# Performance work log

Hardware: AMD Instinct MI355X
Metric: run time of the kernel (lower is better)

The kernel has to match this reference:

```python
import jax, jax.numpy as jnp
import numpy as np

N_NODES = 50000
N_EDGES = 800000
N_GRAPHS = 128
IN_C, HID_C, OUT_C = 128, 256, 128


def setup_inputs() -> dict:
    key = jax.random.key(0)
    ks = jax.random.split(key, 10)
    x = jax.random.normal(ks[0], (N_NODES, IN_C), dtype=jnp.float32)
    edge_index = jax.random.randint(ks[1], (2, N_EDGES), 0, N_NODES, dtype=jnp.int32)
    batch = jnp.sort(jax.random.randint(ks[2], (N_NODES,), 0, N_GRAPHS, dtype=jnp.int32))
    def glorot(k, fan_in, fan_out):
        lim = (6.0 / (fan_in + fan_out)) ** 0.5
        return jax.random.uniform(k, (fan_in, fan_out), jnp.float32, -lim, lim)
    W1 = glorot(ks[3], IN_C, HID_C)
    b1 = jnp.zeros((HID_C,), jnp.float32)
    W2 = glorot(ks[4], HID_C, HID_C)
    b2 = jnp.zeros((HID_C,), jnp.float32)
    Wfc = glorot(ks[5], HID_C, OUT_C)
    bfc = jnp.zeros((OUT_C,), jnp.float32)
    return {"x": x, "edge_index": edge_index, "batch": batch,
            "W1": W1, "b1": b1, "W2": W2, "b2": b2, "Wfc": Wfc, "bfc": bfc}


def _gcn_conv(x, src, dst, W, b, n_nodes):
    # PyG GCNConv: h = x @ W; out[dst] += norm * h[src]; out += b
    h = x @ W  # [N, F_out]
    ones = jnp.ones(src.shape, dtype=h.dtype)
    deg = jax.ops.segment_sum(ones, dst, num_segments=n_nodes)  # in-degree incl self loops
    dinv = jnp.where(deg > 0, jax.lax.rsqrt(deg), 0.0)
    norm = dinv[src] * dinv[dst]                    # [E]
    msg = h[src] * norm[:, None]                    # gather + scale, [E, F_out]
    out = jax.ops.segment_sum(msg, dst, num_segments=n_nodes)  # scatter-add
    return out + b


def reference(x, edge_index, batch, W1, b1, W2, b2, Wfc, bfc):
    n = x.shape[0]
    loops = jnp.arange(n, dtype=edge_index.dtype)
    src = jnp.concatenate([edge_index[0], loops])   # add self loops (GCNConv default)
    dst = jnp.concatenate([edge_index[1], loops])
    h = jax.nn.relu(_gcn_conv(x, src, dst, W1, b1, n))
    h = jax.nn.relu(_gcn_conv(h, src, dst, W2, b2, n))
    # global_mean_pool keyed by batch index
    sums = jax.ops.segment_sum(h, batch, num_segments=N_GRAPHS)          # [G, HID]
    cnts = jax.ops.segment_sum(jnp.ones((n,), h.dtype), batch, num_segments=N_GRAPHS)
    pooled = sums / jnp.maximum(cnts, 1.0)[:, None]
    return pooled @ Wfc + bfc
```

## Files before the change

kernel.cpp:

```cpp
#include <hip/hip_runtime.h>
#include <type_traits>

#define HID 256
#define INC 128
#define OUTC 128

typedef __attribute__((ext_vector_type(8))) short short8;
typedef __attribute__((ext_vector_type(4))) float floatx4;

__device__ __forceinline__ unsigned short f2bf(float f) {
    unsigned int u = __float_as_uint(f);
    unsigned int r = (u + 0x7FFFu + ((u >> 16) & 1u)) >> 16;
    return (unsigned short)r;
}

__device__ __forceinline__ void bfacc2(float* a, uint u, float nr) {
    a[0] = fmaf(nr, __uint_as_float(u << 16), a[0]);
    a[1] = fmaf(nr, __uint_as_float(u & 0xFFFF0000u), a[1]);
}

__global__ void k_hist(const int* __restrict__ dst, int* __restrict__ cnt, int e) {
    int i = blockIdx.x * blockDim.x + threadIdx.x;
    if (i < e) atomicAdd(&cnt[dst[i]], 1);
}

__global__ __launch_bounds__(256) void k_scan_local(const int* __restrict__ cnt,
                                                    int* __restrict__ ex, int* __restrict__ blk_sum,
                                                    float* __restrict__ dinv, int n) {
    __shared__ int s[256];
    const int t = threadIdx.x;
    const int i = blockIdx.x * 256 + t;
    const int v = (i < n) ? cnt[i] : 0;
    if (i < n) dinv[i] = rsqrtf((float)v + 1.0f);
    s[t] = v;
    __syncthreads();
    for (int off = 1; off < 256; off <<= 1) {
        int add = (t >= off) ? s[t - off] : 0;
        __syncthreads();
        s[t] += add;
        __syncthreads();
    }
    if (i < n) ex[i] = s[t] - v;
    if (t == 255) blk_sum[blockIdx.x] = s[255];
}

__global__ __launch_bounds__(256) void k_scan_add(int* __restrict__ row_ptr,
                                                  const int* __restrict__ blk_sum,
                                                  int* __restrict__ cnt, int n, int e) {
    __shared__ int s[256];
    const int t = threadIdx.x;
    const int b = blockIdx.x;
    s[t] = (t < b) ? blk_sum[t] : 0;
    __syncthreads();
    for (int off = 128; off > 0; off >>= 1) {
        if (t < off) s[t] += s[t + off];
        __syncthreads();
    }
    const int offset = s[0];
    const int i = b * 256 + t;
    if (i < n) { row_ptr[i] += offset; cnt[i] = 0; }
    if (i == 0) row_ptr[n] = e;
}

__global__ void k_fill(const int* __restrict__ src, const int* __restrict__ dst,
                       const int* __restrict__ row_ptr, int* __restrict__ cursor,
                       int2* __restrict__ csr, const float* __restrict__ dinv, int e) {
    int i = blockIdx.x * blockDim.x + threadIdx.x;
    if (i < e) {
        const int d = dst[i];
        const int s = src[i];
        const int pos = row_ptr[d] + atomicAdd(&cursor[d], 1);
        csr[pos] = make_int2(s, __float_as_int(dinv[s] * dinv[d]));
    }
}

__global__ void k_conv(const float* __restrict__ x, unsigned short* __restrict__ xb,
                       const float* __restrict__ W1, unsigned short* __restrict__ Wt1,
                       const float* __restrict__ W2, unsigned short* __restrict__ Wt2,
                       int* __restrict__ cnt, float* __restrict__ pooled,
                       int nx4, int n) {
    const int id = blockIdx.x * 256 + threadIdx.x;
    if (id < n) cnt[id] = 0;
    if (id < 128 * HID) pooled[id] = 0.0f;
    if (id < nx4) {
        const float4 v = *(const float4*)(x + (size_t)id * 4);
        uint2 o;
        o.x = (unsigned)f2bf(v.x) | ((unsigned)f2bf(v.y) << 16);
        o.y = (unsigned)f2bf(v.z) | ((unsigned)f2bf(v.w) << 16);
        *(uint2*)(xb + (size_t)id * 4) = o;
        return;
    }
    const int id2 = id - nx4;
    if (id2 < INC * HID) {
        const int nn = id2 / INC;
        const int kk = id2 - nn * INC;
        Wt1[id2] = f2bf(W1[kk * HID + nn]);
        return;
    }
    const int id3 = id2 - INC * HID;
    if (id3 < HID * HID) {
        const int nn = id3 / HID;
        const int kk = id3 - nn * HID;
        Wt2[id3] = f2bf(W2[kk * HID + nn]);
    }
}

template <int CH>
__global__ __launch_bounds__(256) void k_agg(const unsigned short* __restrict__ h,
                                             const int* __restrict__ row_ptr,
                                             const int2* __restrict__ csr,
                                             const float* __restrict__ dinv,
                                             unsigned short* __restrict__ out, int n) {
    constexpr int CPL = CH / 64;
    using VT = std::conditional_t<CPL == 2, uint, uint2>;
    const int v = (blockIdx.x * 256 + threadIdx.x) >> 6;
    const int lane = threadIdx.x & 63;
    if (v >= n) return;
    const float dv = dinv[v];
    const unsigned short* hl = h + lane * CPL;

    float acc[CPL];
    {
        const VT u = *(const VT*)(hl + (size_t)v * CH);
        const float s2 = dv * dv;
        if constexpr (CPL == 2) {
            acc[0] = s2 * __uint_as_float(((uint)u) << 16);
            acc[1] = s2 * __uint_as_float(((uint)u) & 0xFFFF0000u);
        } else {
            const uint2 w = (uint2)u;
            acc[0] = s2 * __uint_as_float(w.x << 16);
            acc[1] = s2 * __uint_as_float(w.x & 0xFFFF0000u);
            acc[2] = s2 * __uint_as_float(w.y << 16);
            acc[3] = s2 * __uint_as_float(w.y & 0xFFFF0000u);
        }
    }

    const int beg = row_ptr[v];
    const int end = row_ptr[v + 1];
    int i = beg;
    for (; i + 4 <= end; i += 4) {
        const int2 p0 = csr[i];
        const int2 p1 = csr[i + 1];
        const int2 p2 = csr[i + 2];
        const int2 p3 = csr[i + 3];
        const float n0 = __int_as_float(p0.y);
        const float n1 = __int_as_float(p1.y);
        const float n2 = __int_as_float(p2.y);
        const float n3 = __int_as_float(p3.y);
        const VT r0 = *(const VT*)(hl + (size_t)p0.x * CH);
        const VT r1 = *(const VT*)(hl + (size_t)p1.x * CH);
        const VT r2 = *(const VT*)(hl + (size_t)p2.x * CH);
        const VT r3 = *(const VT*)(hl + (size_t)p3.x * CH);
        if constexpr (CPL == 2) {
            bfacc2(acc, (uint)r0, n0);
            bfacc2(acc, (uint)r1, n1);
            bfacc2(acc, (uint)r2, n2);
            bfacc2(acc, (uint)r3, n3);
        } else {
            const uint2 w0 = (uint2)r0, w1 = (uint2)r1, w2 = (uint2)r2, w3 = (uint2)r3;
            bfacc2(acc, w0.x, n0); bfacc2(acc + 2, w0.y, n0);
            bfacc2(acc, w1.x, n1); bfacc2(acc + 2, w1.y, n1);
            bfacc2(acc, w2.x, n2); bfacc2(acc + 2, w2.y, n2);
            bfacc2(acc, w3.x, n3); bfacc2(acc + 2, w3.y, n3);
        }
    }
    for (; i < end; ++i) {
        const int2 p0 = csr[i];
        const float n0 = __int_as_float(p0.y);
        const VT r0 = *(const VT*)(hl + (size_t)p0.x * CH);
        if constexpr (CPL == 2) {
            bfacc2(acc, (uint)r0, n0);
        } else {
            const uint2 w0 = (uint2)r0;
            bfacc2(acc, w0.x, n0); bfacc2(acc + 2, w0.y, n0);
        }
    }

    if constexpr (CPL == 2) {
        uint o = (unsigned)f2bf(acc[0]) | ((unsigned)f2bf(acc[1]) << 16);
        *(uint*)(out + (size_t)v * CH + lane * CPL) = o;
    } else {
        uint2 o;
        o.x = (unsigned)f2bf(acc[0]) | ((unsigned)f2bf(acc[1]) << 16);
        o.y = (unsigned)f2bf(acc[2]) | ((unsigned)f2bf(acc[3]) << 16);
        *(uint2*)(out + (size_t)v * CH + lane * CPL) = o;
    }
}

template <int K, bool RELU, bool POOL, typename OT>
__global__ __launch_bounds__(256) void k_gemm_mfma(const unsigned short* __restrict__ A,
                                                   const unsigned short* __restrict__ Wt,
                                                   const float* __restrict__ bias,
                                                   OT* __restrict__ out,
                                                   const int* __restrict__ batch,
                                                   float* __restrict__ pooled_sum, int M) {
    constexpr int LDA = K + 8;
    __shared__ unsigned short sA[32 * LDA];
    __shared__ int s_batch[32];
    const int t = threadIdx.x;
    const int row0 = blockIdx.x * 32;

    {
        const int r = t >> 3;
        const int c0 = (t & 7) * (K / 8);
        unsigned short* dstp = &sA[r * LDA + c0];
        if (row0 + r < M) {
            const unsigned short* srcp = A + (size_t)(row0 + r) * K + c0;
#pragma unroll
            for (int j = 0; j < K / 8; j += 8)
                *(uint4*)(dstp + j) = *(const uint4*)(srcp + j);
        } else {
            const uint4 z = {0, 0, 0, 0};
#pragma unroll
            for (int j = 0; j < K / 8; j += 8) *(uint4*)(dstp + j) = z;
        }
        if constexpr (POOL) {
            if (t < 32) s_batch[t] = (row0 + t < M) ? batch[row0 + t] : -1;
        }
    }
    __syncthreads();

    const int wv = t >> 6;
    const int lane = t & 63;
    const int m16 = lane & 15;
    const int quad = lane >> 4;

    floatx4 acc[2][4];
#pragma unroll
    for (int h2 = 0; h2 < 2; ++h2)
#pragma unroll
        for (int j = 0; j < 4; ++j) acc[h2][j] = (floatx4){0.f, 0.f, 0.f, 0.f};

    const unsigned short* ap0 = &sA[m16 * LDA + quad * 8];
    const unsigned short* ap1 = &sA[(16 + m16) * LDA + quad * 8];
    const unsigned short* bp = Wt + (size_t)(wv * 64 + m16) * K + quad * 8;

#pragma unroll
    for (int k0 = 0; k0 < K; k0 += 32) {
        const short8 a0 = *(const short8*)(ap0 + k0);
        const short8 a1 = *(const short8*)(ap1 + k0);
        const short8 b0 = *(const short8*)(bp + 0 * 16 * K + k0);
        const short8 b1 = *(const short8*)(bp + 1 * 16 * K + k0);
        const short8 b2 = *(const short8*)(bp + 2 * 16 * K + k0);
        const short8 b3 = *(const short8*)(bp + 3 * 16 * K + k0);
        acc[0][0] = __builtin_amdgcn_mfma_f32_16x16x32_bf16(a0, b0, acc[0][0], 0, 0, 0);
        acc[0][1] = __builtin_amdgcn_mfma_f32_16x16x32_bf16(a0, b1, acc[0][1], 0, 0, 0);
        acc[0][2] = __builtin_amdgcn_mfma_f32_16x16x32_bf16(a0, b2, acc[0][2], 0, 0, 0);
        acc[0][3] = __builtin_amdgcn_mfma_f32_16x16x32_bf16(a0, b3, acc[0][3], 0, 0, 0);
        acc[1][0] = __builtin_amdgcn_mfma_f32_16x16x32_bf16(a1, b0, acc[1][0], 0, 0, 0);
        acc[1][1] = __builtin_amdgcn_mfma_f32_16x16x32_bf16(a1, b1, acc[1][1], 0, 0, 0);
        acc[1][2] = __builtin_amdgcn_mfma_f32_16x16x32_bf16(a1, b2, acc[1][2], 0, 0, 0);
        acc[1][3] = __builtin_amdgcn_mfma_f32_16x16x32_bf16(a1, b3, acc[1][3], 0, 0, 0);
    }

    const int nbase = wv * 64 + m16;
    const float bb0 = bias[nbase + 0];
    const float bb1 = bias[nbase + 16];
    const float bb2 = bias[nbase + 32];
    const float bb3 = bias[nbase + 48];

    if constexpr (POOL) {
        float ps0 = 0.f, ps1 = 0.f, ps2 = 0.f, ps3 = 0.f;
        int gcur = -1;
#pragma unroll
        for (int h2 = 0; h2 < 2; ++h2) {
#pragma unroll
            for (int j = 0; j < 4; ++j) {
                const int rl = h2 * 16 + quad * 4 + j;
                const int g = s_batch[rl];
                if (g < 0) continue;
                if (g != gcur) {
                    if (gcur >= 0) {
                        float* pp = pooled_sum + gcur * HID + nbase;
                        atomicAdd(pp + 0, ps0);
                        atomicAdd(pp + 16, ps1);
                        atomicAdd(pp + 32, ps2);
                        atomicAdd(pp + 48, ps3);
                    }
                    ps0 = ps1 = ps2 = ps3 = 0.f;
                    gcur = g;
                }
                ps0 += fmaxf(acc[h2][0][j] + bb0, 0.f);
                ps1 += fmaxf(acc[h2][1][j] + bb1, 0.f);
                ps2 += fmaxf(acc[h2][2][j] + bb2, 0.f);
                ps3 += fmaxf(acc[h2][3][j] + bb3, 0.f);
            }
        }
        if (gcur >= 0) {
            float* pp = pooled_sum + gcur * HID + nbase;
            atomicAdd(pp + 0, ps0);
            atomicAdd(pp + 16, ps1);
            atomicAdd(pp + 32, ps2);
            atomicAdd(pp + 48, ps3);
        }
    } else {
#pragma unroll
        for (int h2 = 0; h2 < 2; ++h2) {
#pragma unroll
            for (int j = 0; j < 4; ++j) {
                const int row = row0 + h2 * 16 + quad * 4 + j;
                if (row >= M) continue;
                float v0 = acc[h2][0][j] + bb0;
                float v1 = acc[h2][1][j] + bb1;
                float v2 = acc[h2][2][j] + bb2;
                float v3 = acc[h2][3][j] + bb3;
                if constexpr (RELU) {
                    v0 = fmaxf(v0, 0.f); v1 = fmaxf(v1, 0.f);
                    v2 = fmaxf(v2, 0.f); v3 = fmaxf(v3, 0.f);
                }
                out[(size_t)row * HID + nbase + 0]  = (OT)f2bf(v0);
                out[(size_t)row * HID + nbase + 16] = (OT)f2bf(v1);
                out[(size_t)row * HID + nbase + 32] = (OT)f2bf(v2);
                out[(size_t)row * HID + nbase + 48] = (OT)f2bf(v3);
            }
        }
    }
}

__global__ void k_fc(const float* __restrict__ pooled_sum, const int* __restrict__ batch,
                     const float* __restrict__ W, const float* __restrict__ b,
                     float* __restrict__ out, int n) {
    const int g = blockIdx.x;
    const int c = threadIdx.x;
    int a = 0, hi = n;
    while (a < hi) { int m = (a + hi) >> 1; if (batch[m] < g) a = m + 1; else hi = m; }
    const int start = a;
    hi = n;
    while (a < hi) { int m = (a + hi) >> 1; if (batch[m] < g + 1) a = m + 1; else hi = m; }
    const float cnt = (float)(a - start);

    float acc = 0.0f;
    const float* p = pooled_sum + g * HID;
    for (int k = 0; k < HID; ++k) acc += p[k] * W[k * OUTC + c];
    out[g * OUTC + c] = acc / fmaxf(cnt, 1.0f) + b[c];
}

extern "C" void kernel_launch(void* const* d_in, const int* in_sizes, int n_in,
                              void* d_out, int out_size, void* d_ws, size_t ws_size,
                              hipStream_t stream) {
    const float* x   = (const float*)d_in[0];
    const int*   ei  = (const int*)d_in[1];
    const int*   bat = (const int*)d_in[2];
    const float* W1  = (const float*)d_in[3];
    const float* b1  = (const float*)d_in[4];
    const float* W2  = (const float*)d_in[5];
    const float* b2  = (const float*)d_in[6];
    const float* Wfc = (const float*)d_in[7];
    const float* bfc = (const float*)d_in[8];
    float* out = (float*)d_out;

    const int n = in_sizes[2];
    const int e = in_sizes[1] / 2;
    const int* src = ei;
    const int* dst = ei + e;
    const int nb = (n + 255) / 256;

    size_t off = 0;
    auto alloc = [&](size_t bytes) {
        char* p = (char*)d_ws + off;
        off += (bytes + 255) & ~(size_t)255;
        return p;
    };
    int*   cnt     = (int*)alloc((size_t)n * 4);
    int*   row_ptr = (int*)alloc((size_t)(n + 1) * 4);
    int*   blk_sum = (int*)alloc(512 * 4);
    int2*  csr     = (int2*)alloc((size_t)e * 8);
    float* dinv    = (float*)alloc((size_t)n * 4);
    unsigned short* Wt1 = (unsigned short*)alloc((size_t)INC * HID * 2);
    unsigned short* Wt2 = (unsigned short*)alloc((size_t)HID * HID * 2);
    unsigned short* R1  = (unsigned short*)alloc((size_t)n * HID * 2);
    unsigned short* R2  = (unsigned short*)alloc((size_t)n * INC * 2);
    unsigned short* R3  = (unsigned short*)alloc((size_t)n * HID * 2);
    float* pooled = (float*)alloc((size_t)128 * HID * 4);

    const int TB = 256;
    const int nx4 = n * INC / 4;

    k_conv<<<(nx4 + INC * HID + HID * HID + TB - 1) / TB, TB, 0, stream>>>(
        x, R1, W1, Wt1, W2, Wt2, cnt, pooled, nx4, n);

    k_hist<<<(e + TB - 1) / TB, TB, 0, stream>>>(dst, cnt, e);
    k_scan_local<<<nb, TB, 0, stream>>>(cnt, row_ptr, blk_sum, dinv, n);
    k_scan_add<<<nb, TB, 0, stream>>>(row_ptr, blk_sum, cnt, n, e);
    k_fill<<<(e + TB - 1) / TB, TB, 0, stream>>>(src, dst, row_ptr, cnt, csr, dinv, e);

    const int gemm_blocks = (n + 31) / 32;
    const int agg_blocks = (n + 3) / 4;

    k_agg<INC><<<agg_blocks, TB, 0, stream>>>(R1, row_ptr, csr, dinv, R2, n);
    k_gemm_mfma<INC, true, false, unsigned short><<<gemm_blocks, TB, 0, stream>>>(
        R2, Wt1, b1, R3, nullptr, nullptr, n);

    k_agg<HID><<<agg_blocks, TB, 0, stream>>>(R3, row_ptr, csr, dinv, R1, n);
    k_gemm_mfma<HID, true, true, float><<<gemm_blocks, TB, 0, stream>>>(
        R1, Wt2, b2, (float*)nullptr, bat, pooled, n);

    k_fc<<<128, 128, 0, stream>>>(pooled, bat, Wfc, bfc, out, n);
}
```

Baseline: 347.2 us.

## Use half-wave aggregation and persistent register-resident-weight MFMA GEMM

The aggregation kernel now assigns 32 lanes per node with wider vector loads, and handles the edge tail with clamped, zero-weighted padded iterations instead of a scalar remainder loop. The GEMM becomes a persistent grid of 512 blocks, each loading its weight fragments into registers once and looping over row tiles. A fragments are read directly from global memory rather than staged through shared memory, which removes the block-wide sync. This cuts per-tile reloads of the weights and the LDS traffic, at the cost of more register pressure (launch bounds 256,2) and uncoalesced direct A loads.

```diff
diff --git a/kernel.cpp b/kernel.cpp
--- a/kernel.cpp
+++ b/kernel.cpp
@@ -111,207 +111,215 @@
                                              const int2* __restrict__ csr,
                                              const float* __restrict__ dinv,
                                              unsigned short* __restrict__ out, int n) {
-    constexpr int CPL = CH / 64;
-    using VT = std::conditional_t<CPL == 2, uint, uint2>;
-    const int v = (blockIdx.x * 256 + threadIdx.x) >> 6;
-    const int lane = threadIdx.x & 63;
+    constexpr int CPL = CH / 32;
+    using VT = std::conditional_t<CPL == 4, uint2, uint4>;
+    const int v = (blockIdx.x * 256 + threadIdx.x) >> 5;
+    const int l = threadIdx.x & 31;
     if (v >= n) return;
     const float dv = dinv[v];
-    const unsigned short* hl = h + lane * CPL;
+    const unsigned short* hl = h + l * CPL;
 
     float acc[CPL];
     {
         const VT u = *(const VT*)(hl + (size_t)v * CH);
         const float s2 = dv * dv;
-        if constexpr (CPL == 2) {
-            acc[0] = s2 * __uint_as_float(((uint)u) << 16);
-            acc[1] = s2 * __uint_as_float(((uint)u) & 0xFFFF0000u);
-        } else {
+        if constexpr (CPL == 4) {
             const uint2 w = (uint2)u;
             acc[0] = s2 * __uint_as_float(w.x << 16);
             acc[1] = s2 * __uint_as_float(w.x & 0xFFFF0000u);
             acc[2] = s2 * __uint_as_float(w.y << 16);
             acc[3] = s2 * __uint_as_float(w.y & 0xFFFF0000u);
+        } else {
+            const uint4 w = (uint4)u;
+            acc[0] = s2 * __uint_as_float(w.x << 16);
+            acc[1] = s2 * __uint_as_float(w.x & 0xFFFF0000u);
+            acc[2] = s2 * __uint_as_float(w.y << 16);
+            acc[3] = s2 * __uint_as_float(w.y & 0xFFFF0000u);
+            acc[4] = s2 * __uint_as_float(w.z << 16);
+            acc[5] = s2 * __uint_as_float(w.z & 0xFFFF0000u);
+            acc[6] = s2 * __uint_as_float(w.w << 16);
+            acc[7] = s2 * __uint_as_float(w.w & 0xFFFF0000u);
         }
     }
 
     const int beg = row_ptr[v];
     const int end = row_ptr[v + 1];
-    int i = beg;
-    for (; i + 4 <= end; i += 4) {
+    for (int i = beg; i < end; i += 4) {
+        const int e1 = min(i + 1, end - 1);
+        const int e2 = min(i + 2, end - 1);
+        const int e3 = min(i + 3, end - 1);
         const int2 p0 = csr[i];
-        const int2 p1 = csr[i + 1];
-        const int2 p2 = csr[i + 2];
-        const int2 p3 = csr[i + 3];
+        const int2 p1 = csr[e1];
+        const int2 p2 = csr[e2];
+        const int2 p3 = csr[e3];
         const float n0 = __int_as_float(p0.y);
-        const float n1 = __int_as_float(p1.y);
-        const float n2 = __int_as_float(p2.y);
-        const float n3 = __int_as_float(p3.y);
+        const float n1 = (i + 1 < end) ? __int_as_float(p1.y) : 0.0f;
+        const float n2 = (i + 2 < end) ? __int_as_float(p2.y) : 0.0f;
+        const float n3 = (i + 3 < end) ? __int_as_float(p3.y) : 0.0f;
         const VT r0 = *(const VT*)(hl + (size_t)p0.x * CH);
         const VT r1 = *(const VT*)(hl + (size_t)p1.x * CH);
         const VT r2 = *(const VT*)(hl + (size_t)p2.x * CH);
         const VT r3 = *(const VT*)(hl + (size_t)p3.x * CH);
-        if constexpr (CPL == 2) {
-            bfacc2(acc, (uint)r0, n0);
-            bfacc2(acc, (uint)r1, n1);
-            bfacc2(acc, (uint)r2, n2);
-            bfacc2(acc, (uint)r3, n3);
-        } else {
+        if constexpr (CPL == 4) {
             const uint2 w0 = (uint2)r0, w1 = (uint2)r1, w2 = (uint2)r2, w3 = (uint2)r3;
             bfacc2(acc, w0.x, n0); bfacc2(acc + 2, w0.y, n0);
             bfacc2(acc, w1.x, n1); bfacc2(acc + 2, w1.y, n1);
             bfacc2(acc, w2.x, n2); bfacc2(acc + 2, w2.y, n2);
             bfacc2(acc, w3.x, n3); bfacc2(acc + 2, w3.y, n3);
+        } else {
+            const uint4 w0 = (uint4)r0, w1 = (uint4)r1, w2 = (uint4)r2, w3 = (uint4)r3;
+            bfacc2(acc, w0.x, n0); bfacc2(acc + 2, w0.y, n0);
+            bfacc2(acc + 4, w0.z, n0); bfacc2(acc + 6, w0.w, n0);
+            bfacc2(acc, w1.x, n1); bfacc2(acc + 2, w1.y, n1);
+            bfacc2(acc + 4, w1.z, n1); bfacc2(acc + 6, w1.w, n1);
+            bfacc2(acc, w2.x, n2); bfacc2(acc + 2, w2.y, n2);
+            bfacc2(acc + 4, w2.z, n2); bfacc2(acc + 6, w2.w, n2);
+            bfacc2(acc, w3.x, n3); bfacc2(acc + 2, w3.y, n3);
+            bfacc2(acc + 4, w3.z, n3); bfacc2(acc + 6, w3.w, n3);
         }
     }
-    for (; i < end; ++i) {
-        const int2 p0 = csr[i];
-        const float n0 = __int_as_float(p0.y);
-        const VT r0 = *(const VT*)(hl + (size_t)p0.x * CH);
-        if constexpr (CPL == 2) {
-            bfacc2(acc, (uint)r0, n0);
-        } else {
-            const uint2 w0 = (uint2)r0;
-            bfacc2(acc, w0.x, n0); bfacc2(acc + 2, w0.y, n0);
-        }
-    }
-
-    if constexpr (CPL == 2) {
-        uint o = (unsigned)f2bf(acc[0]) | ((unsigned)f2bf(acc[1]) << 16);
-        *(uint*)(out + (size_t)v * CH + lane * CPL) = o;
-    } else {
+
+    if constexpr (CPL == 4) {
         uint2 o;
         o.x = (unsigned)f2bf(acc[0]) | ((unsigned)f2bf(acc[1]) << 16);
         o.y = (unsigned)f2bf(acc[2]) | ((unsigned)f2bf(acc[3]) << 16);
-        *(uint2*)(out + (size_t)v * CH + lane * CPL) = o;
+        *(uint2*)(out + (size_t)v * CH + l * 4) = o;
+    } else {
+        uint4 o;
+        o.x = (unsigned)f2bf(acc[0]) | ((unsigned)f2bf(acc[1]) << 16);
+        o.y = (unsigned)f2bf(acc[2]) | ((unsigned)f2bf(acc[3]) << 16);
+        o.z = (unsigned)f2bf(acc[4]) | ((unsigned)f2bf(acc[5]) << 16);
+        o.w = (unsigned)f2bf(acc[6]) | ((unsigned)f2bf(acc[7]) << 16);
+        *(uint4*)(out + (size_t)v * CH + l * 8) = o;
     }
 }
 
 template <int K, bool RELU, bool POOL, typename OT>
-__global__ __launch_bounds__(256) void k_gemm_mfma(const unsigned short* __restrict__ A,
+__global__ __launch_bounds__(256, 2) void k_gemm_p(const unsigned short* __restrict__ A,
                                                    const unsigned short* __restrict__ Wt,
                                                    const float* __restrict__ bias,
                                                    OT* __restrict__ out,
                                                    const int* __restrict__ batch,
-                                                   float* __restrict__ pooled_sum, int M) {
-    constexpr int LDA = K + 8;
-    __shared__ unsigned short sA[32 * LDA];
-    __shared__ int s_batch[32];
+                                                   float* __restrict__ pooled_sum,
+                                                   int M, int ntiles) {
     const int t = threadIdx.x;
-    const int row0 = blockIdx.x * 32;
-
-    {
-        const int r = t >> 3;
-        const int c0 = (t & 7) * (K / 8);
-        unsigned short* dstp = &sA[r * LDA + c0];
-        if (row0 + r < M) {
-            const unsigned short* srcp = A + (size_t)(row0 + r) * K + c0;
-#pragma unroll
-            for (int j = 0; j < K / 8; j += 8)
-                *(uint4*)(dstp + j) = *(const uint4*)(srcp + j);
-        } else {
-            const uint4 z = {0, 0, 0, 0};
-#pragma unroll
-            for (int j = 0; j < K / 8; j += 8) *(uint4*)(dstp + j) = z;
-        }
-        if constexpr (POOL) {
-            if (t < 32) s_batch[t] = (row0 + t < M) ? batch[row0 + t] : -1;
-        }
-    }
-    __syncthreads();
-
     const int wv = t >> 6;
     const int lane = t & 63;
     const int m16 = lane & 15;
     const int quad = lane >> 4;
-
-    floatx4 acc[2][4];
-#pragma unroll
-    for (int h2 = 0; h2 < 2; ++h2)
-#pragma unroll
-        for (int j = 0; j < 4; ++j) acc[h2][j] = (floatx4){0.f, 0.f, 0.f, 0.f};
-
-    const unsigned short* ap0 = &sA[m16 * LDA + quad * 8];
-    const unsigned short* ap1 = &sA[(16 + m16) * LDA + quad * 8];
-    const unsigned short* bp = Wt + (size_t)(wv * 64 + m16) * K + quad * 8;
-
-#pragma unroll
-    for (int k0 = 0; k0 < K; k0 += 32) {
-        const short8 a0 = *(const short8*)(ap0 + k0);
-        const short8 a1 = *(const short8*)(ap1 + k0);
-        const short8 b0 = *(const short8*)(bp + 0 * 16 * K + k0);
-        const short8 b1 = *(const short8*)(bp + 1 * 16 * K + k0);
-        const short8 b2 = *(const short8*)(bp + 2 * 16 * K + k0);
-        const short8 b3 = *(const short8*)(bp + 3 * 16 * K + k0);
-        acc[0][0] = __builtin_amdgcn_mfma_f32_16x16x32_bf16(a0, b0, acc[0][0], 0, 0, 0);
-        acc[0][1] = __builtin_amdgcn_mfma_f32_16x16x32_bf16(a0, b1, acc[0][1], 0, 0, 0);
-        acc[0][2] = __builtin_amdgcn_mfma_f32_16x16x32_bf16(a0, b2, acc[0][2], 0, 0, 0);
-        acc[0][3] = __builtin_amdgcn_mfma_f32_16x16x32_bf16(a0, b3, acc[0][3], 0, 0, 0);
-        acc[1][0] = __builtin_amdgcn_mfma_f32_16x16x32_bf16(a1, b0, acc[1][0], 0, 0, 0);
-        acc[1][1] = __builtin_amdgcn_mfma_f32_16x16x32_bf16(a1, b1, acc[1][1], 0, 0, 0);
-        acc[1][2] = __builtin_amdgcn_mfma_f32_16x16x32_bf16(a1, b2, acc[1][2], 0, 0, 0);
-        acc[1][3] = __builtin_amdgcn_mfma_f32_16x16x32_bf16(a1, b3, acc[1][3], 0, 0, 0);
-    }
-
     const int nbase = wv * 64 + m16;
+
+    short8 Bf[4][K / 32];
+    {
+        const unsigned short* bp = Wt + (size_t)nbase * K + quad * 8;
+#pragma unroll
+        for (int nt = 0; nt < 4; ++nt)
+#pragma unroll
+            for (int ks = 0; ks < K / 32; ++ks)
+                Bf[nt][ks] = *(const short8*)(bp + nt * 16 * K + ks * 32);
+    }
     const float bb0 = bias[nbase + 0];
     const float bb1 = bias[nbase + 16];
     const float bb2 = bias[nbase + 32];
     const float bb3 = bias[nbase + 48];
-
-    if constexpr (POOL) {
-        float ps0 = 0.f, ps1 = 0.f, ps2 = 0.f, ps3 = 0.f;
-        int gcur = -1;
-#pragma unroll
-        for (int h2 = 0; h2 < 2; ++h2) {
-#pragma unroll
-            for (int j = 0; j < 4; ++j) {
-                const int rl = h2 * 16 + quad * 4 + j;
-                const int g = s_batch[rl];
-                if (g < 0) continue;
-                if (g != gcur) {
-                    if (gcur >= 0) {
-                        float* pp = pooled_sum + gcur * HID + nbase;
-                        atomicAdd(pp + 0, ps0);
-                        atomicAdd(pp + 16, ps1);
-                        atomicAdd(pp + 32, ps2);
-                        atomicAdd(pp + 48, ps3);
-                    }
-                    ps0 = ps1 = ps2 = ps3 = 0.f;
-                    gcur = g;
-                }
-                ps0 += fmaxf(acc[h2][0][j] + bb0, 0.f);
-                ps1 += fmaxf(acc[h2][1][j] + bb1, 0.f);
-                ps2 += fmaxf(acc[h2][2][j] + bb2, 0.f);
-                ps3 += fmaxf(acc[h2][3][j] + bb3, 0.f);
+    const short8 z8 = {0, 0, 0, 0, 0, 0, 0, 0};
+
+    for (int tile = blockIdx.x; tile < ntiles; tile += gridDim.x) {
+        const int row0 = tile * 32;
+        floatx4 acc[2][4];
+#pragma unroll
+        for (int h2 = 0; h2 < 2; ++h2)
+#pragma unroll
+            for (int j = 0; j < 4; ++j) acc[h2][j] = (floatx4){0.f, 0.f, 0.f, 0.f};
+
+        const unsigned short* ar0 = A + (size_t)(row0 + m16) * K + quad * 8;
+        if (row0 + 32 <= M) {
+#pragma unroll
+            for (int ks = 0; ks < K / 32; ++ks) {
+                const short8 a0 = *(const short8*)(ar0 + ks * 32);
+                const short8 a1 = *(const short8*)(ar0 + 16 * K + ks * 32);
+                acc[0][0] = __builtin_amdgcn_mfma_f32_16x16x32_bf16(a0, Bf[0][ks], acc[0][0], 0, 0, 0);
+                acc[0][1] = __builtin_amdgcn_mfma_f32_16x16x32_bf16(a0, Bf[1][ks], acc[0][1], 0, 0, 0);
+                acc[0][2] = __builtin_amdgcn_mfma_f32_16x16x32_bf16(a0, Bf[2][ks], acc[0][2], 0, 0, 0);
+                acc[0][3] = __builtin_amdgcn_mfma_f32_16x16x32_bf16(a0, Bf[3][ks], acc[0][3], 0, 0, 0);
+                acc[1][0] = __builtin_amdgcn_mfma_f32_16x16x32_bf16(a1, Bf[0][ks], acc[1][0], 0, 0, 0);
+                acc[1][1] = __builtin_amdgcn_mfma_f32_16x16x32_bf16(a1, Bf[1][ks], acc[1][1], 0, 0, 0);
+                acc[1][2] = __builtin_amdgcn_mfma_f32_16x16x32_bf16(a1, Bf[2][ks], acc[1][2], 0, 0, 0);
+                acc[1][3] = __builtin_amdgcn_mfma_f32_16x16x32_bf16(a1, Bf[3][ks], acc[1][3], 0, 0, 0);
+            }
+        } else {
+            const bool r0ok = (row0 + m16) < M;
+            const bool r1ok = (row0 + 16 + m16) < M;
+#pragma unroll
+            for (int ks = 0; ks < K / 32; ++ks) {
+                short8 a0 = z8, a1 = z8;
+                if (r0ok) a0 = *(const short8*)(ar0 + ks * 32);
+                if (r1ok) a1 = *(const short8*)(ar0 + 16 * K + ks * 32);
+                acc[0][0] = __builtin_amdgcn_mfma_f32_16x16x32_bf16(a0, Bf[0][ks], acc[0][0], 0, 0, 0);
+                acc[0][1] = __builtin_amdgcn_mfma_f32_16x16x32_bf16(a0, Bf[1][ks], acc[0][1], 0, 0, 0);
+                acc[0][2] = __builtin_amdgcn_mfma_f32_16x16x32_bf16(a0, Bf[2][ks], acc[0][2], 0, 0, 0);
+                acc[0][3] = __builtin_amdgcn_mfma_f32_16x16x32_bf16(a0, Bf[3][ks], acc[0][3], 0, 0, 0);
+                acc[1][0] = __builtin_amdgcn_mfma_f32_16x16x32_bf16(a1, Bf[0][ks], acc[1][0], 0, 0, 0);
+                acc[1][1] = __builtin_amdgcn_mfma_f32_16x16x32_bf16(a1, Bf[1][ks], acc[1][1], 0, 0, 0);
+                acc[1][2] = __builtin_amdgcn_mfma_f32_16x16x32_bf16(a1, Bf[2][ks], acc[1][2], 0, 0, 0);
+                acc[1][3] = __builtin_amdgcn_mfma_f32_16x16x32_bf16(a1, Bf[3][ks], acc[1][3], 0, 0, 0);
             }
         }
-        if (gcur >= 0) {
-            float* pp = pooled_sum + gcur * HID + nbase;
-            atomicAdd(pp + 0, ps0);
-            atomicAdd(pp + 16, ps1);
-            atomicAdd(pp + 32, ps2);
-            atomicAdd(pp + 48, ps3);
-        }
-    } else {
-#pragma unroll
-        for (int h2 = 0; h2 < 2; ++h2) {
-#pragma unroll
-            for (int j = 0; j < 4; ++j) {
-                const int row = row0 + h2 * 16 + quad * 4 + j;
-                if (row >= M) continue;
-                float v0 = acc[h2][0][j] + bb0;
-                float v1 = acc[h2][1][j] + bb1;
-                float v2 = acc[h2][2][j] + bb2;
-                float v3 = acc[h2][3][j] + bb3;
-                if constexpr (RELU) {
-                    v0 = fmaxf(v0, 0.f); v1 = fmaxf(v1, 0.f);
-                    v2 = fmaxf(v2, 0.f); v3 = fmaxf(v3, 0.f);
+
+        if constexpr (POOL) {
+            float ps0 = 0.f, ps1 = 0.f, ps2 = 0.f, ps3 = 0.f;
+            int gcur = -1;
+#pragma unroll
+            for (int h2 = 0; h2 < 2; ++h2) {
+#pragma unroll
+                for (int j = 0; j < 4; ++j) {
+                    const int row = row0 + h2 * 16 + quad * 4 + j;
+                    const int g = (row < M) ? batch[row] : -1;
+                    if (g < 0) continue;
+                    if (g != gcur) {
+                        if (gcur >= 0) {
+                            float* pp = pooled_sum + gcur * HID + nbase;
+                            atomicAdd(pp + 0, ps0);
+                            atomicAdd(pp + 16, ps1);
+                            atomicAdd(pp + 32, ps2);
+                            atomicAdd(pp + 48, ps3);
+                        }
+                        ps0 = ps1 = ps2 = ps3 = 0.f;
+                        gcur = g;
+                    }
+                    ps0 += fmaxf(acc[h2][0][j] + bb0, 0.f);
+                    ps1 += fmaxf(acc[h2][1][j] + bb1, 0.f);
+                    ps2 += fmaxf(acc[h2][2][j] + bb2, 0.f);
+                    ps3 += fmaxf(acc[h2][3][j] + bb3, 0.f);
                 }
-                out[(size_t)row * HID + nbase + 0]  = (OT)f2bf(v0);
-                out[(size_t)row * HID + nbase + 16] = (OT)f2bf(v1);
-                out[(size_t)row * HID + nbase + 32] = (OT)f2bf(v2);
-                out[(size_t)row * HID + nbase + 48] = (OT)f2bf(v3);
+            }
+            if (gcur >= 0) {
+                float* pp = pooled_sum + gcur * HID + nbase;
+                atomicAdd(pp + 0, ps0);
+                atomicAdd(pp + 16, ps1);
+                atomicAdd(pp + 32, ps2);
+                atomicAdd(pp + 48, ps3);
+            }
+        } else {
+#pragma unroll
+            for (int h2 = 0; h2 < 2; ++h2) {
+#pragma unroll
+                for (int j = 0; j < 4; ++j) {
+                    const int row = row0 + h2 * 16 + quad * 4 + j;
+                    if (row >= M) continue;
+                    float v0 = acc[h2][0][j] + bb0;
+                    float v1 = acc[h2][1][j] + bb1;
+                    float v2 = acc[h2][2][j] + bb2;
+                    float v3 = acc[h2][3][j] + bb3;
+                    if constexpr (RELU) {
+                        v0 = fmaxf(v0, 0.f); v1 = fmaxf(v1, 0.f);
+                        v2 = fmaxf(v2, 0.f); v3 = fmaxf(v3, 0.f);
+                    }
+                    out[(size_t)row * HID + nbase + 0]  = (OT)f2bf(v0);
+                    out[(size_t)row * HID + nbase + 16] = (OT)f2bf(v1);
+                    out[(size_t)row * HID + nbase + 32] = (OT)f2bf(v2);
+                    out[(size_t)row * HID + nbase + 48] = (OT)f2bf(v3);
+                }
             }
         }
     }
@@ -384,16 +392,17 @@
     k_scan_add<<<nb, TB, 0, stream>>>(row_ptr, blk_sum, cnt, n, e);
     k_fill<<<(e + TB - 1) / TB, TB, 0, stream>>>(src, dst, row_ptr, cnt, csr, dinv, e);
 
-    const int gemm_blocks = (n + 31) / 32;
-    const int agg_blocks = (n + 3) / 4;
+    const int ntiles = (n + 31) / 32;
+    const int agg_blocks = (n + 7) / 8;
+    const int GEMM_GRID = 512;
 
     k_agg<INC><<<agg_blocks, TB, 0, stream>>>(R1, row_ptr, csr, dinv, R2, n);
-    k_gemm_mfma<INC, true, false, unsigned short><<<gemm_blocks, TB, 0, stream>>>(
-        R2, Wt1, b1, R3, nullptr, nullptr, n);
+    k_gemm_p<INC, true, false, unsigned short><<<GEMM_GRID, TB, 0, stream>>>(
+        R2, Wt1, b1, R3, nullptr, nullptr, n, ntiles);
 
     k_agg<HID><<<agg_blocks, TB, 0, stream>>>(R3, row_ptr, csr, dinv, R1, n);
-    k_gemm_mfma<HID, true, true, float><<<gemm_blocks, TB, 0, stream>>>(
-        R1, Wt2, b2, (float*)nullptr, bat, pooled, n);
+    k_gemm_p<HID, true, true, float><<<GEMM_GRID, TB, 0, stream>>>(
+        R1, Wt2, b2, (float*)nullptr, bat, pooled, n, ntiles);
 
     k_fc<<<128, 128, 0, stream>>>(pooled, bat, Wfc, bfc, out, n);
 }
```

Result: faster. 338.7 us (-2.4%).
